# Optimization experiments

Measured on AMD Instinct MI355X. Metric: run time of the kernel, lower is better.

Reference implementation:

```python
import jax, jax.numpy as jnp
import numpy as np

N = 50000      # nodes
E = 800000     # edges
G = 256        # graphs in batch
D_IN = 128     # input_dim
H = 128        # node_hidden_dim
FC = 128       # fc_hidden_dim
OUT = 2        # out_dim
EPS = 1e-5


def _lin_init(key, fan_in, fan_out, bias=True):
    kw, kb = jax.random.split(key)
    w = jax.random.normal(kw, (fan_in, fan_out), jnp.float32) / np.sqrt(fan_in)
    if bias:
        b = jax.random.normal(kb, (fan_out,), jnp.float32) * 0.01
        return w, b
    return w


def setup_inputs() -> dict:
    key = jax.random.key(0)
    ks = jax.random.split(key, 16)
    x = jax.random.normal(ks[0], (N, D_IN), jnp.float32)
    edge_index = jax.random.randint(ks[1], (2, E), 0, N, jnp.int32)
    batch = jnp.sort(jax.random.randint(ks[2], (N,), 0, G, jnp.int32))
    edge_attr = jax.random.uniform(ks[3], (E, 1), jnp.float32)
    # GraphConv params: lin_rel (with bias) + lin_root (no bias)
    w_rel1, b_rel1 = _lin_init(ks[4], D_IN, H)
    w_root1 = _lin_init(ks[5], D_IN, H, bias=False)
    w_rel2, b_rel2 = _lin_init(ks[6], H, 2 * H)
    w_root2 = _lin_init(ks[7], H, 2 * H, bias=False)
    w_rel3, b_rel3 = _lin_init(ks[8], 2 * H, 3 * H)
    w_root3 = _lin_init(ks[9], 2 * H, 3 * H, bias=False)
    # BatchNorm affine params
    gamma1 = jnp.ones((H,), jnp.float32);      beta1 = jnp.zeros((H,), jnp.float32)
    gamma2 = jnp.ones((2 * H,), jnp.float32);  beta2 = jnp.zeros((2 * H,), jnp.float32)
    gamma3 = jnp.ones((3 * H,), jnp.float32);  beta3 = jnp.zeros((3 * H,), jnp.float32)
    # FC head: lin1 in = 3H+6H+9H = 18H
    w_lin1, b_lin1 = _lin_init(ks[10], 18 * H, FC)
    w_lin2, b_lin2 = _lin_init(ks[11], FC, OUT)
    w_lin3, b_lin3 = _lin_init(ks[12], OUT, OUT)
    return dict(x=x, edge_index=edge_index, batch=batch, edge_attr=edge_attr,
                w_rel1=w_rel1, b_rel1=b_rel1, w_root1=w_root1,
                w_rel2=w_rel2, b_rel2=b_rel2, w_root2=w_root2,
                w_rel3=w_rel3, b_rel3=b_rel3, w_root3=w_root3,
                gamma1=gamma1, beta1=beta1, gamma2=gamma2, beta2=beta2,
                gamma3=gamma3, beta3=beta3,
                w_lin1=w_lin1, b_lin1=b_lin1, w_lin2=w_lin2, b_lin2=b_lin2,
                w_lin3=w_lin3, b_lin3=b_lin3)


def _bn(h, gamma, beta):
    # training-mode BatchNorm1d over node axis
    mu = h.mean(0)
    var = h.var(0)
    return (h - mu) * jax.lax.rsqrt(var + EPS) * gamma + beta


def _gconv(h, src, dst, ew, w_rel, b_rel, w_root):
    # PyG GraphConv: lin_rel(sum_j ew_ij * x_j) + lin_root(x_i)
    agg = jax.ops.segment_sum(h[src] * ew[:, None], dst, num_segments=N)
    return agg @ w_rel + b_rel + h @ w_root


def _pool3(h, batch):
    # concat of global max / mean / add pooling per graph
    s = jax.ops.segment_sum(h, batch, num_segments=G)
    cnt = jax.ops.segment_sum(jnp.ones((h.shape[0], 1), h.dtype), batch, num_segments=G)
    mean = s / jnp.maximum(cnt, 1.0)
    m = jax.ops.segment_max(h, batch, num_segments=G)
    m = jnp.where(cnt > 0, m, 0.0)  # guard empty segments
    return jnp.concatenate([m, mean, s], axis=1)


def reference(x, edge_index, batch, edge_attr,
              w_rel1, b_rel1, w_root1, w_rel2, b_rel2, w_root2,
              w_rel3, b_rel3, w_root3,
              gamma1, beta1, gamma2, beta2, gamma3, beta3,
              w_lin1, b_lin1, w_lin2, b_lin2, w_lin3, b_lin3):
    ew = jnp.transpose(edge_attr, (1, 0))[0]            # [E]
    src, dst = edge_index[0], edge_index[1]
    h = _bn(jax.nn.leaky_relu(_gconv(x, src, dst, ew, w_rel1, b_rel1, w_root1)), gamma1, beta1)
    x1 = _pool3(h, batch)
    h = _bn(jax.nn.leaky_relu(_gconv(h, src, dst, ew, w_rel2, b_rel2, w_root2)), gamma2, beta2)
    x2 = _pool3(h, batch)
    h = _bn(jax.nn.leaky_relu(_gconv(h, src, dst, ew, w_rel3, b_rel3, w_root3)), gamma3, beta3)
    x3 = _pool3(h, batch)
    z = jnp.concatenate([x1, x2, x3], axis=1)           # [G, 18H]
    z = jax.nn.relu(z @ w_lin1 + b_lin1)                # dropout is identity in eval
    z = jax.nn.relu(z @ w_lin2 + b_lin2)
    return jax.nn.log_softmax(z @ w_lin3 + b_lin3, axis=-1)
```

## Files before the change

### kernel.cpp

```cpp
#include <hip/hip_runtime.h>
#include <cstdint>
#include <cstddef>

#define N_NODES 50000
#define M_PAD   50048
#define MB_TILES 391
#define N_EDGES 800000
#define N_GRAPH 256
#define Z_DIM   2304
#define NREP    16
#define POOL_TOT (N_GRAPH * (128 + 256 + 384))
#define PP_L1 (MB_TILES * 1 * 2 * 2 * 128)
#define PP_L2 (MB_TILES * 2 * 2 * 2 * 128)
#define PP_L3 (MB_TILES * 3 * 2 * 2 * 128)
#define PP_TOT (PP_L1 + PP_L2 + PP_L3)

static constexpr float LEAKY  = 0.01f;
static constexpr float BN_EPS = 1e-5f;
static constexpr float FNEG   = -3.4e38f;
static constexpr float FPOS   =  3.4e38f;

typedef short short8 __attribute__((ext_vector_type(8)));
typedef float floatx4 __attribute__((ext_vector_type(4)));
typedef const __attribute__((address_space(1))) unsigned int* gas_ptr;
typedef __attribute__((address_space(3))) unsigned int* las_ptr;
typedef unsigned long long ull;

__device__ __forceinline__ unsigned short f2b(float f) {
  union { float f; unsigned int u; } v; v.f = f;
  unsigned int u = v.u;
  unsigned int r = (u + 0x7FFFu + ((u >> 16) & 1u)) >> 16;
  return (unsigned short)r;
}
__device__ __forceinline__ float b2f(unsigned short h) {
  union { unsigned int u; float f; } v; v.u = ((unsigned int)h) << 16;
  return v.f;
}
__device__ __forceinline__ unsigned fkey(float x) {
  unsigned k = __float_as_uint(x);
  return k ^ ((k & 0x80000000u) ? 0xFFFFFFFFu : 0x80000000u);
}
__device__ __forceinline__ float kdec(unsigned k) {
  k ^= (k & 0x80000000u) ? 0x80000000u : 0xFFFFFFFFu;
  return __uint_as_float(k);
}


__global__ void init_all_kernel(int* __restrict__ cntR, int* __restrict__ gcnt,
                                float* __restrict__ sums_all,
                                unsigned* __restrict__ pmaxk, unsigned* __restrict__ pmink,
                                float* __restrict__ psumg) {
  const int i = blockIdx.x * blockDim.x + threadIdx.x;
  if (i < NREP * N_NODES) cntR[i] = 0;
  if (i < N_GRAPH) gcnt[i] = 0;
  if (i < 2 * (128 + 256 + 384)) sums_all[i] = 0.f;
  if (i < POOL_TOT) { pmaxk[i] = 0u; pmink[i] = 0xFFFFFFFFu; psumg[i] = 0.f; }
}


__global__ void hist_rep_kernel(const int* __restrict__ idx, int* __restrict__ cntR, int n) {
  int i = blockIdx.x * blockDim.x + threadIdx.x;
  if (i < n) {
    const int rep = blockIdx.x & (NREP - 1);
    atomicAdd(&cntR[rep * N_NODES + idx[i]], 1);
  }
}

__global__ __launch_bounds__(256) void scan1_fused_kernel(int* __restrict__ cntR,
                                                          int* __restrict__ out,
                                                          int* __restrict__ part, int n) {
  __shared__ int sm[256];
  const int t = threadIdx.x;
  const int base = blockIdx.x * 1024 + t * 4;
  int v[4] = {0, 0, 0, 0};
#pragma unroll
  for (int j = 0; j < 4; ++j) {
    const int d = base + j;
    if (d < n) {
      int s = 0;
#pragma unroll
      for (int r = 0; r < NREP; ++r) {
        const int c = cntR[r * N_NODES + d];
        cntR[r * N_NODES + d] = s;
        s += c;
      }
      v[j] = s;
    }
  }
  const int tsum = v[0] + v[1] + v[2] + v[3];
  sm[t] = tsum;
  __syncthreads();
  for (int off = 1; off < 256; off <<= 1) {
    int x = (t >= off) ? sm[t - off] : 0;
    __syncthreads();
    sm[t] += x;
    __syncthreads();
  }
  const int excl = sm[t] - tsum;
  if (base     < n) out[base]     = excl;
  if (base + 1 < n) out[base + 1] = excl + v[0];
  if (base + 2 < n) out[base + 2] = excl + v[0] + v[1];
  if (base + 3 < n) out[base + 3] = excl + v[0] + v[1] + v[2];
  if (t == 255) part[blockIdx.x] = sm[255];
}

__global__ __launch_bounds__(256) void scan2_kernel(int* __restrict__ part, int nb,
                                                    int* __restrict__ total_out) {
  __shared__ int sm[256];
  const int t = threadIdx.x;
  const int v = (t < nb) ? part[t] : 0;
  sm[t] = v;
  __syncthreads();
  for (int off = 1; off < 256; off <<= 1) {
    int x = (t >= off) ? sm[t - off] : 0;
    __syncthreads();
    sm[t] += x;
    __syncthreads();
  }
  if (t < nb) part[t] = sm[t] - v;
  if (t == 255) *total_out = sm[255];
}

__global__ void scan3_cursor_kernel(int* __restrict__ out, const int* __restrict__ part,
                                    int* __restrict__ cntR, int n) {
  int i = blockIdx.x * blockDim.x + threadIdx.x;
  if (i >= n) return;
  const int rp = out[i] + part[i >> 10];
  out[i] = rp;
#pragma unroll
  for (int r = 0; r < NREP; ++r) cntR[r * N_NODES + i] += rp;
}

__global__ void bucket_kernel(const int* __restrict__ src, const int* __restrict__ dst,
                              const float* __restrict__ ew, int* __restrict__ cntR,
                              ull* __restrict__ epack, int E) {
  int e = blockIdx.x * blockDim.x + threadIdx.x;
  if (e < E) {
    const int rep = blockIdx.x & (NREP - 1);
    const int d = dst[e];
    const int p = atomicAdd(&cntR[rep * N_NODES + d], 1);
    epack[p] = ((ull)__float_as_uint(ew[e]) << 32) | (unsigned)src[e];
  }
}

__global__ __launch_bounds__(256) void hist_batch_kernel(const int* __restrict__ idx,
                                                         int* __restrict__ cnt, int n) {
  __shared__ int lh[N_GRAPH];
  lh[threadIdx.x] = 0;
  __syncthreads();
  int i = blockIdx.x * blockDim.x + threadIdx.x;
  if (i < n) atomicAdd(&lh[idx[i]], 1);
  __syncthreads();
  const int v = lh[threadIdx.x];
  if (v) atomicAdd(&cnt[threadIdx.x], v);
}

__global__ __launch_bounds__(256) void scan256_kernel(const int* __restrict__ cnt,
                                                      int* __restrict__ gptr) {
  __shared__ int sm[256];
  const int t = threadIdx.x;
  const int v = cnt[t];
  sm[t] = v;
  __syncthreads();
  for (int off = 1; off < 256; off <<= 1) {
    int x = (t >= off) ? sm[t - off] : 0;
    __syncthreads();
    sm[t] += x;
    __syncthreads();
  }
  gptr[t] = sm[t] - v;
  if (t == 255) gptr[256] = sm[255];
}


__global__ void cast_bf16_kernel(const float* __restrict__ in,
                                 unsigned short* __restrict__ out, int npair) {
  int i = blockIdx.x * blockDim.x + threadIdx.x;
  if (i >= npair) return;
  float2 v = *(const float2*)(in + 2 * (size_t)i);
  ((unsigned int*)out)[i] = (unsigned int)f2b(v.x) | ((unsigned int)f2b(v.y) << 16);
}

__global__ __launch_bounds__(256) void wt_build_kernel(
    const float* __restrict__ wrel, const float* __restrict__ wroot,
    const float* __restrict__ brel, const float* __restrict__ sums_prev,
    const float* __restrict__ gamma_prev, const float* __restrict__ beta_prev,
    unsigned short* __restrict__ wt, float* __restrict__ u, float* __restrict__ v,
    int K, int N) {
  __shared__ float redu[256];
  __shared__ float redv[256];
  const int n = blockIdx.x;
  const int K2 = 2 * K;
  const float inv_n = 1.f / (float)N_NODES;
  float us = 0.f, vs = 0.f;
  for (int k = threadIdx.x; k < K2; k += 256) {
    const int kk = (k < K) ? k : k - K;
    const float w = (k < K) ? wrel[(size_t)kk * N + n] : wroot[(size_t)kk * N + n];
    float sc = 1.f, sh = 0.f;
    if (sums_prev) {
      const float mu  = sums_prev[kk] * inv_n;
      const float var = sums_prev[K + kk] * inv_n - mu * mu;
      sc = rsqrtf(var + BN_EPS) * gamma_prev[kk];
      sh = beta_prev[kk] - mu * sc;
    }
    wt[(size_t)n * K2 + k] = f2b(w * sc);
    if (k < K) us += sh * w; else vs += sh * w;
  }
  redu[threadIdx.x] = us; redv[threadIdx.x] = vs;
  __syncthreads();
  for (int o = 128; o > 0; o >>= 1) {
    if (threadIdx.x < o) {
      redu[threadIdx.x] += redu[threadIdx.x + o];
      redv[threadIdx.x] += redv[threadIdx.x + o];
    }
    __syncthreads();
  }
  if (threadIdx.x == 0) { u[n] = redu[0]; v[n] = brel[n] + redv[0]; }
}


template <int D>
__global__ void agg_bf16_kernel(const unsigned short* __restrict__ h,
                                const int* __restrict__ rowptr,
                                const ull* __restrict__ epack,
                                unsigned short* __restrict__ agg,
                                float* __restrict__ degw_out) {
  int gid  = blockIdx.x * blockDim.x + threadIdx.x;
  int node = gid >> 6;
  int lane = threadIdx.x & 63;
  if (node >= N_NODES) return;
  const int beg = rowptr[node], end = rowptr[node + 1];
  constexpr int NP = D / 128;
  float acc0[NP], acc1[NP];
#pragma unroll
  for (int i = 0; i < NP; ++i) { acc0[i] = 0.f; acc1[i] = 0.f; }
  float wsum = 0.f;

  for (int c0 = beg; c0 < end; c0 += 64) {
    const int cn = min(64, end - c0);
    ull pk = 0;
    if (lane < cn) pk = epack[c0 + lane];
    const int   su = (int)(unsigned)pk;
    const float wf = __uint_as_float((unsigned)(pk >> 32));
    const int ng = (cn + 7) >> 3;
    for (int g = 0; g < ng; ++g) {
      int ss[8]; float wv[8];
#pragma unroll
      for (int j = 0; j < 8; ++j) {
        ss[j] = __shfl(su, g * 8 + j);
        wv[j] = __shfl(wf, g * 8 + j);
      }
      unsigned uu[8][NP];
#pragma unroll
      for (int j = 0; j < 8; ++j) {
        const unsigned int* row = (const unsigned int*)(h + (size_t)ss[j] * D);
#pragma unroll
        for (int i = 0; i < NP; ++i) uu[j][i] = row[lane + 64 * i];
      }
#pragma unroll
      for (int j = 0; j < 8; ++j) {
        wsum += wv[j];
#pragma unroll
        for (int i = 0; i < NP; ++i) {
          acc0[i] += b2f((unsigned short)(uu[j][i] & 0xFFFF)) * wv[j];
          acc1[i] += b2f((unsigned short)(uu[j][i] >> 16)) * wv[j];
        }
      }
    }
  }

  unsigned int* o = (unsigned int*)(agg + (size_t)node * D);
#pragma unroll
  for (int i = 0; i < NP; ++i)
    o[lane + 64 * i] = (unsigned int)f2b(acc0[i]) | ((unsigned int)f2b(acc1[i]) << 16);
  if (degw_out != nullptr && lane == 0) degw_out[node] = wsum;
}


__global__ __launch_bounds__(256) void gemm_mfma_kernel(
    const unsigned short* __restrict__ Aagg, const unsigned short* __restrict__ Ah,
    const unsigned short* __restrict__ Wt,
    const float* __restrict__ u, const float* __restrict__ v,
    const float* __restrict__ degw, const int* __restrict__ batch,
    unsigned short* __restrict__ outH, float* __restrict__ sums,
    unsigned* __restrict__ pmaxk, unsigned* __restrict__ pmink,
    float* __restrict__ psumg,
    float* __restrict__ ppmax, float* __restrict__ ppmin, float* __restrict__ ppsum,
    int M, int K, int N) {
  __shared__ unsigned short As[3][128 * 32];
  __shared__ unsigned short Bs[3][128 * 32];
  __shared__ float col_s[256];
  __shared__ float dws[128];
  __shared__ int gbs[128];

  const int NT = N >> 7;
  const int id = blockIdx.x;
  const int xcd = id & 7;
  const int q   = id >> 3;
  const int m_tile = (q / NT) * 8 + xcd;
  if (m_tile >= MB_TILES) return;
  const int m0 = m_tile * 128;
  const int nt2 = q % NT;
  const int n0 = nt2 * 128;

  const int t  = threadIdx.x;
  const int lane = t & 63;
  const int w    = t >> 6;
  const int wm   = (w & 1) * 64;
  const int wn   = (w >> 1) * 64;
  const int l16  = lane & 15;
  const int lq   = lane >> 4;
  const int K2   = 2 * K;

  const int lrow  = lane >> 2;
  const int lslot = lane & 3;

  col_s[t] = 0.f;
  if (t < 128) {
    const int m = m0 + t;
    dws[t] = (m < M) ? degw[m] : 0.f;
    gbs[t] = (m < M) ? batch[m] : -1;
  }

  floatx4 acc[4][4];
#pragma unroll
  for (int i = 0; i < 4; ++i)
#pragma unroll
    for (int j = 0; j < 4; ++j) acc[i][j] = (floatx4){0.f, 0.f, 0.f, 0.f};

  auto stage = [&](unsigned short* Ab, unsigned short* Bb, int k0) {
    const unsigned short* Asrc;
    int kbase;
    if (k0 < K) { Asrc = Aagg; kbase = k0; } else { Asrc = Ah; kbase = k0 - K; }
#pragma unroll
    for (int qq = 0; qq < 2; ++qq) {
      const int row = w * 32 + qq * 16 + lrow;
      const int gc  = (lslot ^ ((row >> 1) & 3)) * 8;
      const unsigned short* gA = Asrc + (size_t)(m0 + row) * K + kbase + gc;
      const unsigned short* gB = Wt + (size_t)(n0 + row) * K2 + k0 + gc;
      __builtin_amdgcn_global_load_lds((gas_ptr)gA, (las_ptr)(Ab + (w * 32 + qq * 16) * 32),
                                       16, 0, 0);
      __builtin_amdgcn_global_load_lds((gas_ptr)gB, (las_ptr)(Bb + (w * 32 + qq * 16) * 32),
                                       16, 0, 0);
    }
  };

  auto compute = [&](const unsigned short* Ab, const unsigned short* Bb) {
    short8 af[4], bfr[4];
#pragma unroll
    for (int i = 0; i < 4; ++i) {
      const int r = wm + i * 16 + l16;
      af[i] = *(const short8*)(Ab + r * 32 + (lq ^ ((r >> 1) & 3)) * 8);
    }
#pragma unroll
    for (int j = 0; j < 4; ++j) {
      const int r = wn + j * 16 + l16;
      bfr[j] = *(const short8*)(Bb + r * 32 + (lq ^ ((r >> 1) & 3)) * 8);
    }
    __builtin_amdgcn_s_setprio(1);
#pragma unroll
    for (int i = 0; i < 4; ++i)
#pragma unroll
      for (int j = 0; j < 4; ++j)
        acc[i][j] = __builtin_amdgcn_mfma_f32_16x16x32_bf16(af[i], bfr[j], acc[i][j], 0, 0, 0);
    __builtin_amdgcn_s_setprio(0);
  };

  const int NSTEP = K2 >> 5;

  unsigned short *A0 = &As[0][0], *A1 = &As[1][0], *A2 = &As[2][0];
  unsigned short *B0 = &Bs[0][0], *B1 = &Bs[1][0], *B2 = &Bs[2][0];

  stage(A0, B0, 0);
  stage(A1, B1, 1 << 5);

  for (int s = 0; s < NSTEP - 1; ++s) {
    asm volatile("s_waitcnt vmcnt(4)" ::: "memory");
    __builtin_amdgcn_s_barrier();
    __builtin_amdgcn_sched_barrier(0);
    if (s + 2 < NSTEP) stage(A2, B2, (s + 2) << 5);
    compute(A0, B0);
    unsigned short* tA = A0; A0 = A1; A1 = A2; A2 = tA;
    unsigned short* tB = B0; B0 = B1; B1 = B2; B2 = tB;
  }
  asm volatile("s_waitcnt vmcnt(0)" ::: "memory");
  __builtin_amdgcn_s_barrier();
  __builtin_amdgcn_sched_barrier(0);
  compute(A0, B0);

  float uu[4], vv[4];
#pragma unroll
  for (int j = 0; j < 4; ++j) {
    const int n = n0 + wn + j * 16 + l16;
    uu[j] = u[n]; vv[j] = v[n];
  }

  const bool wout = (outH != nullptr);
  const int lastr = min(127, M - 1 - m0);
  const int gmin = gbs[0];
  const int gmax = gbs[lastr];

  float ts[4]  = {0.f, 0.f, 0.f, 0.f};
  float tss[4] = {0.f, 0.f, 0.f, 0.f};
  float px0[4], pn0[4], ps0[4], px1[4], pn1[4], ps1[4];
#pragma unroll
  for (int j = 0; j < 4; ++j) {
    px0[j] = FNEG; pn0[j] = FPOS; ps0[j] = 0.f;
    px1[j] = FNEG; pn1[j] = FPOS; ps1[j] = 0.f;
  }

#pragma unroll
  for (int i = 0; i < 4; ++i) {
    const int lrow2 = wm + i * 16 + lq * 4;
#pragma unroll
    for (int r = 0; r < 4; ++r) {
      const int row = lrow2 + r;
      const bool live = (m0 + row < M);
      const int gv = gbs[row];
      const float dwr = dws[row];
      const bool in0 = live && (gv == gmin);
      const bool in1 = live && (gmax != gmin) && (gv == gmax);
#pragma unroll
      for (int j = 0; j < 4; ++j) {
        const int n = n0 + wn + j * 16 + l16;
        float val = acc[i][j][r] + vv[j] + dwr * uu[j];
        val = val > 0.f ? val : LEAKY * val;
        acc[i][j][r] = val;
        if (live) {
          if (wout) outH[(size_t)(m0 + row) * N + n] = f2b(val);
          ts[j]  += val;
          tss[j] += val * val;
        }
        if (in0) { px0[j] = fmaxf(px0[j], val); pn0[j] = fminf(pn0[j], val); ps0[j] += val; }
        if (in1) { px1[j] = fmaxf(px1[j], val); pn1[j] = fminf(pn1[j], val); ps1[j] += val; }
      }
    }
  }

  const int half = w & 1;
#pragma unroll
  for (int j = 0; j < 4; ++j) {
    float a = ts[j], b = tss[j];
    a += __shfl_xor(a, 16); a += __shfl_xor(a, 32);
    b += __shfl_xor(b, 16); b += __shfl_xor(b, 32);
    float x0 = px0[j], n0v = pn0[j], s0v = ps0[j];
    x0 = fmaxf(x0, __shfl_xor(x0, 16)); x0 = fmaxf(x0, __shfl_xor(x0, 32));
    n0v = fminf(n0v, __shfl_xor(n0v, 16)); n0v = fminf(n0v, __shfl_xor(n0v, 32));
    s0v += __shfl_xor(s0v, 16); s0v += __shfl_xor(s0v, 32);
    float x1 = px1[j], n1v = pn1[j], s1v = ps1[j];
    x1 = fmaxf(x1, __shfl_xor(x1, 16)); x1 = fmaxf(x1, __shfl_xor(x1, 32));
    n1v = fminf(n1v, __shfl_xor(n1v, 16)); n1v = fminf(n1v, __shfl_xor(n1v, 32));
    s1v += __shfl_xor(s1v, 16); s1v += __shfl_xor(s1v, 32);
    if (lq == 0) {
      const int ci = wn + j * 16 + l16;
      atomicAdd(&col_s[ci], a);
      atomicAdd(&col_s[128 + ci], b);
      const size_t tb = (size_t)(m_tile * NT + nt2) * 2;
      const size_t sb0 = ((tb + 0) * 2 + half) * 128 + ci;
      const size_t sb1 = ((tb + 1) * 2 + half) * 128 + ci;
      ppmax[sb0] = x0;  ppmin[sb0] = n0v; ppsum[sb0] = s0v;
      ppmax[sb1] = x1;  ppmin[sb1] = n1v; ppsum[sb1] = s1v;
    }
  }

  if (gmax > gmin + 1) {
    for (int g = gmin + 1; g < gmax; ++g) {
#pragma unroll
      for (int j = 0; j < 4; ++j) {
        float mx = FNEG, mn = FPOS, sm = 0.f;
#pragma unroll
        for (int i = 0; i < 4; ++i) {
          const int lrow2 = wm + i * 16 + lq * 4;
#pragma unroll
          for (int r = 0; r < 4; ++r) {
            const int row = lrow2 + r;
            if (m0 + row < M && gbs[row] == g) {
              const float val = acc[i][j][r];
              mx = fmaxf(mx, val); mn = fminf(mn, val); sm += val;
            }
          }
        }
        mx = fmaxf(mx, __shfl_xor(mx, 16)); mx = fmaxf(mx, __shfl_xor(mx, 32));
        mn = fminf(mn, __shfl_xor(mn, 16)); mn = fminf(mn, __shfl_xor(mn, 32));
        sm += __shfl_xor(sm, 16); sm += __shfl_xor(sm, 32);
        if (lq == 0 && mx > -3.3e38f) {
          const size_t pi = (size_t)g * N + (n0 + wn + j * 16 + l16);
          atomicMax(&pmaxk[pi], fkey(mx));
          atomicMin(&pmink[pi], fkey(mn));
          atomicAdd(&psumg[pi], sm);
        }
      }
    }
  }

  __syncthreads();
  if (t < 128) {
    atomicAdd(&sums[n0 + t], col_s[t]);
    atomicAdd(&sums[N + n0 + t], col_s[128 + t]);
  }
}


__global__ void pool_finalize_all_kernel(const unsigned* __restrict__ pmaxk,
                                         const unsigned* __restrict__ pmink,
                                         const float* __restrict__ psumg,
                                         const float* __restrict__ ppmax,
                                         const float* __restrict__ ppmin,
                                         const float* __restrict__ ppsum,
                                         const float* __restrict__ sums_all,
                                         const float* __restrict__ gamma1, const float* __restrict__ beta1,
                                         const float* __restrict__ gamma2, const float* __restrict__ beta2,
                                         const float* __restrict__ gamma3, const float* __restrict__ beta3,
                                         const int* __restrict__ gptr,
                                         const int* __restrict__ batch,
                                         float* __restrict__ z) {
  int i = blockIdx.x * blockDim.x + threadIdx.x;
  if (i >= POOL_TOT) return;
  int C, zoff, li, NTL;
  size_t ppo;
  const float *sums, *gamma, *beta;
  if (i < N_GRAPH * 128) {
    C = 128; zoff = 0; li = i; NTL = 1; ppo = 0;
    sums = sums_all; gamma = gamma1; beta = beta1;
  } else if (i < N_GRAPH * (128 + 256)) {
    C = 256; zoff = 384; li = i - N_GRAPH * 128; NTL = 2; ppo = PP_L1;
    sums = sums_all + 2 * 128; gamma = gamma2; beta = beta2;
  } else {
    C = 384; zoff = 1152; li = i - N_GRAPH * (128 + 256); NTL = 3; ppo = PP_L1 + PP_L2;
    sums = sums_all + 2 * (128 + 256); gamma = gamma3; beta = beta3;
  }
  const int g = li / C, c = li % C;
  const int cnt = gptr[g + 1] - gptr[g];

  float mx = FNEG, mn = FPOS, sm = psumg[i];
  {
    const unsigned pk = pmaxk[i];
    if (pk != 0u) mx = kdec(pk);
    const unsigned nk = pmink[i];
    if (nk != 0xFFFFFFFFu) mn = kdec(nk);
  }
  if (cnt > 0) {
    const int mt_lo = gptr[g] >> 7;
    const int mt_hi = (gptr[g + 1] - 1) >> 7;
    const int nt = c >> 7, cc = c & 127;
    for (int mt = mt_lo; mt <= mt_hi; ++mt) {
      const int g0 = batch[mt << 7];
      int grel = (g == g0) ? 0 : -1;
      if (grel < 0) {
        const int lastm = min((mt << 7) + 127, N_NODES - 1);
        if (g == batch[lastm]) grel = 1;
      }
      if (grel >= 0) {
        const size_t b0 = ppo + (((size_t)(mt * NTL + nt) * 2 + grel) * 2 + 0) * 128 + cc;
        const size_t b1 = b0 + 128;
        mx = fmaxf(mx, fmaxf(ppmax[b0], ppmax[b1]));
        mn = fminf(mn, fminf(ppmin[b0], ppmin[b1]));
        sm += ppsum[b0] + ppsum[b1];
      }
    }
  }

  const float inv_n = 1.f / (float)N_NODES;
  const float mu  = sums[c] * inv_n;
  const float var = sums[C + c] * inv_n - mu * mu;
  const float sc  = rsqrtf(var + BN_EPS) * gamma[c];
  const float sh  = beta[c] - mu * sc;
  const float zmax = (sc >= 0.f ? mx : mn) * sc + sh;
  const float zsum = sm * sc + (float)cnt * sh;
  float* zg = z + (size_t)g * Z_DIM + zoff;
  zg[c]         = (cnt > 0) ? zmax : 0.f;
  zg[C + c]     = zsum / (float)(cnt > 0 ? cnt : 1);
  zg[2 * C + c] = zsum;
}


__global__ __launch_bounds__(1024) void fc_kernel(const float* __restrict__ z,
                                                  const float* __restrict__ w1, const float* __restrict__ b1,
                                                  const float* __restrict__ w2, const float* __restrict__ b2,
                                                  const float* __restrict__ w3, const float* __restrict__ b3,
                                                  float* __restrict__ out) {
  __shared__ float zs[Z_DIM];
  __shared__ float part[8][128];
  __shared__ float h1s[128];
  __shared__ float red[128][2];
  __shared__ float y2[2];
  const int g  = blockIdx.x;
  const int t  = threadIdx.x;
  const int c  = t & 127;
  const int ks = t >> 7;
  for (int i = t; i < Z_DIM; i += 1024) zs[i] = z[(size_t)g * Z_DIM + i];
  __syncthreads();

  constexpr int KCH = Z_DIM / 8;
  const int k0 = ks * KCH;
  float acc = 0.f;
#pragma unroll 4
  for (int k = k0; k < k0 + KCH; ++k) acc += zs[k] * w1[(size_t)k * 128 + c];
  part[ks][c] = acc;
  __syncthreads();

  if (t < 128) {
    float s = b1[t];
#pragma unroll
    for (int i = 0; i < 8; ++i) s += part[i][t];
    h1s[t] = fmaxf(s, 0.f);
  }
  __syncthreads();
  if (t < 128) {
    red[t][0] = h1s[t] * w2[t * 2 + 0];
    red[t][1] = h1s[t] * w2[t * 2 + 1];
  }
  __syncthreads();
  if (t < 2) {
    float s = b2[t];
    for (int k = 0; k < 128; ++k) s += red[k][t];
    y2[t] = fmaxf(s, 0.f);
  }
  __syncthreads();
  if (t == 0) {
    const float z0 = y2[0] * w3[0] + y2[1] * w3[2] + b3[0];
    const float z1 = y2[0] * w3[1] + y2[1] * w3[3] + b3[1];
    const float m  = fmaxf(z0, z1);
    const float lse = m + logf(expf(z0 - m) + expf(z1 - m));
    out[g * 2 + 0] = z0 - lse;
    out[g * 2 + 1] = z1 - lse;
  }
}


extern "C" void kernel_launch(void* const* d_in, const int* in_sizes, int n_in,
                              void* d_out, int out_size, void* d_ws, size_t ws_size,
                              hipStream_t stream) {
  (void)in_sizes; (void)n_in; (void)out_size; (void)ws_size;
  const float* x        = (const float*)d_in[0];
  const int*   eidx     = (const int*)d_in[1];
  const int*   batch    = (const int*)d_in[2];
  const float* eattr    = (const float*)d_in[3];
  const float* w_rel1   = (const float*)d_in[4];
  const float* b_rel1   = (const float*)d_in[5];
  const float* w_root1  = (const float*)d_in[6];
  const float* w_rel2   = (const float*)d_in[7];
  const float* b_rel2   = (const float*)d_in[8];
  const float* w_root2  = (const float*)d_in[9];
  const float* w_rel3   = (const float*)d_in[10];
  const float* b_rel3   = (const float*)d_in[11];
  const float* w_root3  = (const float*)d_in[12];
  const float* gamma1   = (const float*)d_in[13];
  const float* beta1    = (const float*)d_in[14];
  const float* gamma2   = (const float*)d_in[15];
  const float* beta2    = (const float*)d_in[16];
  const float* gamma3   = (const float*)d_in[17];
  const float* beta3    = (const float*)d_in[18];
  const float* w_lin1   = (const float*)d_in[19];
  const float* b_lin1   = (const float*)d_in[20];
  const float* w_lin2   = (const float*)d_in[21];
  const float* b_lin2   = (const float*)d_in[22];
  const float* w_lin3   = (const float*)d_in[23];
  const float* b_lin3   = (const float*)d_in[24];

  const int* src = eidx;
  const int* dst = eidx + N_EDGES;
  float* outp = (float*)d_out;

  char* ws = (char*)d_ws;
  size_t off = 0;
  auto alloc = [&](size_t bytes) -> void* {
    void* p = ws + off;
    off += (bytes + 255) & ~(size_t)255;
    return p;
  };
  int*   rowptr = (int*)alloc((N_NODES + 1) * sizeof(int));
  int*   cntR   = (int*)alloc((size_t)NREP * N_NODES * sizeof(int));
  int*   gptr   = (int*)alloc((N_GRAPH + 1) * sizeof(int));
  int*   gcnt   = (int*)alloc(N_GRAPH * sizeof(int));
  int*   part   = (int*)alloc(256 * sizeof(int));
  ull*   epack  = (ull*)alloc((size_t)N_EDGES * sizeof(ull));
  float* degw   = (float*)alloc(N_NODES * sizeof(float));
  float* sums_all = (float*)alloc(2 * (128 + 256 + 384) * sizeof(float));
  float* zbuf   = (float*)alloc((size_t)N_GRAPH * Z_DIM * sizeof(float));
  unsigned* pmaxk = (unsigned*)alloc((size_t)POOL_TOT * 4);
  unsigned* pmink = (unsigned*)alloc((size_t)POOL_TOT * 4);
  float*    psumg = (float*)alloc((size_t)POOL_TOT * 4);
  float* ppmax = (float*)alloc((size_t)PP_TOT * 4);
  float* ppmin = (float*)alloc((size_t)PP_TOT * 4);
  float* ppsum = (float*)alloc((size_t)PP_TOT * 4);
  unsigned short* xb   = (unsigned short*)alloc((size_t)M_PAD * 128 * 2);
  unsigned short* hp1  = (unsigned short*)alloc((size_t)M_PAD * 128 * 2);
  unsigned short* hp2  = (unsigned short*)alloc((size_t)M_PAD * 256 * 2);
  unsigned short* aggb = (unsigned short*)alloc((size_t)M_PAD * 256 * 2);
  unsigned short* wt1 = (unsigned short*)alloc((size_t)128 * 256 * 2);
  unsigned short* wt2 = (unsigned short*)alloc((size_t)256 * 256 * 2);
  unsigned short* wt3 = (unsigned short*)alloc((size_t)384 * 512 * 2);
  float* u1 = (float*)alloc(128 * sizeof(float));
  float* v1 = (float*)alloc(128 * sizeof(float));
  float* u2 = (float*)alloc(256 * sizeof(float));
  float* v2 = (float*)alloc(256 * sizeof(float));
  float* u3 = (float*)alloc(384 * sizeof(float));
  float* v3 = (float*)alloc(384 * sizeof(float));

  float* sums1 = sums_all;
  float* sums2 = sums_all + 2 * 128;
  float* sums3 = sums_all + 2 * (128 + 256);
  const int PO1 = 0, PO2 = N_GRAPH * 128, PO3 = N_GRAPH * (128 + 256);

  const int EB = (N_EDGES + 255) / 256;
  const int NB = (N_NODES + 255) / 256;
  const int SB = (N_NODES + 1023) / 1024;

  init_all_kernel<<<(NREP * N_NODES + 255) / 256, 256, 0, stream>>>(
      cntR, gcnt, sums_all, pmaxk, pmink, psumg);

  hist_rep_kernel<<<EB, 256, 0, stream>>>(dst, cntR, N_EDGES);
  scan1_fused_kernel<<<SB, 256, 0, stream>>>(cntR, rowptr, part, N_NODES);
  scan2_kernel<<<1, 256, 0, stream>>>(part, SB, rowptr + N_NODES);
  scan3_cursor_kernel<<<NB, 256, 0, stream>>>(rowptr, part, cntR, N_NODES);
  bucket_kernel<<<EB, 256, 0, stream>>>(src, dst, eattr, cntR, epack, N_EDGES);

  hist_batch_kernel<<<NB, 256, 0, stream>>>(batch, gcnt, N_NODES);
  scan256_kernel<<<1, 256, 0, stream>>>(gcnt, gptr);

  cast_bf16_kernel<<<(N_NODES * 128 / 2 + 255) / 256, 256, 0, stream>>>(x, xb, N_NODES * 128 / 2);
  wt_build_kernel<<<128, 256, 0, stream>>>(w_rel1, w_root1, b_rel1, nullptr, nullptr, nullptr,
                                           wt1, u1, v1, 128, 128);

  const int aggBlocks = (N_NODES * 64 + 255) / 256;

  agg_bf16_kernel<128><<<aggBlocks, 256, 0, stream>>>(xb, rowptr, epack, aggb, degw);
  gemm_mfma_kernel<<<392 * 1, 256, 0, stream>>>(aggb, xb, wt1, u1, v1, degw, batch,
                                                hp1, sums1, pmaxk + PO1, pmink + PO1,
                                                psumg + PO1, ppmax, ppmin, ppsum,
                                                N_NODES, 128, 128);
  wt_build_kernel<<<256, 256, 0, stream>>>(w_rel2, w_root2, b_rel2, sums1, gamma1, beta1,
                                           wt2, u2, v2, 128, 256);

  agg_bf16_kernel<128><<<aggBlocks, 256, 0, stream>>>(hp1, rowptr, epack, aggb, nullptr);
  gemm_mfma_kernel<<<392 * 2, 256, 0, stream>>>(aggb, hp1, wt2, u2, v2, degw, batch,
                                                hp2, sums2, pmaxk + PO2, pmink + PO2,
                                                psumg + PO2, ppmax + PP_L1, ppmin + PP_L1,
                                                ppsum + PP_L1, N_NODES, 128, 256);
  wt_build_kernel<<<384, 256, 0, stream>>>(w_rel3, w_root3, b_rel3, sums2, gamma2, beta2,
                                           wt3, u3, v3, 256, 384);

  agg_bf16_kernel<256><<<aggBlocks, 256, 0, stream>>>(hp2, rowptr, epack, aggb, nullptr);
  gemm_mfma_kernel<<<392 * 3, 256, 0, stream>>>(aggb, hp2, wt3, u3, v3, degw, batch,
                                                (unsigned short*)nullptr, sums3,
                                                pmaxk + PO3, pmink + PO3, psumg + PO3,
                                                ppmax + PP_L1 + PP_L2, ppmin + PP_L1 + PP_L2,
                                                ppsum + PP_L1 + PP_L2, N_NODES, 256, 384);

  pool_finalize_all_kernel<<<(POOL_TOT + 255) / 256, 256, 0, stream>>>(
      pmaxk, pmink, psumg, ppmax, ppmin, ppsum, sums_all,
      gamma1, beta1, gamma2, beta2, gamma3, beta3, gptr, batch, zbuf);
  fc_kernel<<<N_GRAPH, 1024, 0, stream>>>(zbuf, w_lin1, b_lin1, w_lin2, b_lin2, w_lin3, b_lin3,
                                          outp);
}
```

Before: 502.7 us.

## Load GEMM fragments directly from global into registers, drop LDS staging

The MFMA GEMM no longer stages A and B tiles through a triple-buffered LDS pipeline with global_load_lds and barriers. Each wave now loads its short8 fragments straight from global memory into registers, double-buffered in software, and sets a launch-bounds occupancy hint of 3. This removes LDS traffic and per-step barriers and frees LDS for more resident blocks. In exchange, rows shared between waves are loaded redundantly, the global accesses are less coalesced, and register pressure rises, which may cap occupancy. A __syncthreads was also added after the shared-memory init, fixing a latent race left when the loop barriers were removed.

```diff
diff --git a/kernel.cpp b/kernel.cpp
--- a/kernel.cpp
+++ b/kernel.cpp
@@ -22,8 +22,6 @@
 
 typedef short short8 __attribute__((ext_vector_type(8)));
 typedef float floatx4 __attribute__((ext_vector_type(4)));
-typedef const __attribute__((address_space(1))) unsigned int* gas_ptr;
-typedef __attribute__((address_space(3))) unsigned int* las_ptr;
 typedef unsigned long long ull;
 
 __device__ __forceinline__ unsigned short f2b(float f) {
@@ -277,7 +275,7 @@
 }
 
 
-__global__ __launch_bounds__(256) void gemm_mfma_kernel(
+__global__ __launch_bounds__(256, 3) void gemm_mfma_kernel(
     const unsigned short* __restrict__ Aagg, const unsigned short* __restrict__ Ah,
     const unsigned short* __restrict__ Wt,
     const float* __restrict__ u, const float* __restrict__ v,
@@ -287,8 +285,6 @@
     float* __restrict__ psumg,
     float* __restrict__ ppmax, float* __restrict__ ppmin, float* __restrict__ ppsum,
     int M, int K, int N) {
-  __shared__ unsigned short As[3][128 * 32];
-  __shared__ unsigned short Bs[3][128 * 32];
   __shared__ float col_s[256];
   __shared__ float dws[128];
   __shared__ int gbs[128];
@@ -312,15 +308,13 @@
   const int lq   = lane >> 4;
   const int K2   = 2 * K;
 
-  const int lrow  = lane >> 2;
-  const int lslot = lane & 3;
-
   col_s[t] = 0.f;
   if (t < 128) {
     const int m = m0 + t;
     dws[t] = (m < M) ? degw[m] : 0.f;
     gbs[t] = (m < M) ? batch[m] : -1;
   }
+  __syncthreads();
 
   floatx4 acc[4][4];
 #pragma unroll
@@ -328,65 +322,42 @@
 #pragma unroll
     for (int j = 0; j < 4; ++j) acc[i][j] = (floatx4){0.f, 0.f, 0.f, 0.f};
 
-  auto stage = [&](unsigned short* Ab, unsigned short* Bb, int k0) {
-    const unsigned short* Asrc;
-    int kbase;
-    if (k0 < K) { Asrc = Aagg; kbase = k0; } else { Asrc = Ah; kbase = k0 - K; }
-#pragma unroll
-    for (int qq = 0; qq < 2; ++qq) {
-      const int row = w * 32 + qq * 16 + lrow;
-      const int gc  = (lslot ^ ((row >> 1) & 3)) * 8;
-      const unsigned short* gA = Asrc + (size_t)(m0 + row) * K + kbase + gc;
-      const unsigned short* gB = Wt + (size_t)(n0 + row) * K2 + k0 + gc;
-      __builtin_amdgcn_global_load_lds((gas_ptr)gA, (las_ptr)(Ab + (w * 32 + qq * 16) * 32),
-                                       16, 0, 0);
-      __builtin_amdgcn_global_load_lds((gas_ptr)gB, (las_ptr)(Bb + (w * 32 + qq * 16) * 32),
-                                       16, 0, 0);
-    }
+  const unsigned short* ApA = Aagg + (size_t)(m0 + wm + l16) * K + lq * 8;
+  const unsigned short* ApH = Ah   + (size_t)(m0 + wm + l16) * K + lq * 8;
+  const unsigned short* Bp  = Wt   + (size_t)(n0 + wn + l16) * K2 + lq * 8;
+
+  short8 afA[4], bfA[4], afB[4], bfB[4];
+
+  auto loadf = [&](short8* af, short8* bf, int s) {
+    const int k0 = s << 5;
+    const unsigned short* Ap = (k0 < K) ? (ApA + k0) : (ApH + (k0 - K));
+#pragma unroll
+    for (int i = 0; i < 4; ++i)
+      af[i] = *(const short8*)(Ap + (size_t)(i * 16) * K);
+    const unsigned short* Bq = Bp + k0;
+#pragma unroll
+    for (int j = 0; j < 4; ++j)
+      bf[j] = *(const short8*)(Bq + (size_t)(j * 16) * K2);
   };
-
-  auto compute = [&](const unsigned short* Ab, const unsigned short* Bb) {
-    short8 af[4], bfr[4];
-#pragma unroll
-    for (int i = 0; i < 4; ++i) {
-      const int r = wm + i * 16 + l16;
-      af[i] = *(const short8*)(Ab + r * 32 + (lq ^ ((r >> 1) & 3)) * 8);
-    }
-#pragma unroll
-    for (int j = 0; j < 4; ++j) {
-      const int r = wn + j * 16 + l16;
-      bfr[j] = *(const short8*)(Bb + r * 32 + (lq ^ ((r >> 1) & 3)) * 8);
-    }
+  auto mf16 = [&](short8* af, short8* bf) {
     __builtin_amdgcn_s_setprio(1);
 #pragma unroll
     for (int i = 0; i < 4; ++i)
 #pragma unroll
       for (int j = 0; j < 4; ++j)
-        acc[i][j] = __builtin_amdgcn_mfma_f32_16x16x32_bf16(af[i], bfr[j], acc[i][j], 0, 0, 0);
+        acc[i][j] = __builtin_amdgcn_mfma_f32_16x16x32_bf16(af[i], bf[j], acc[i][j], 0, 0, 0);
     __builtin_amdgcn_s_setprio(0);
   };
 
   const int NSTEP = K2 >> 5;
 
-  unsigned short *A0 = &As[0][0], *A1 = &As[1][0], *A2 = &As[2][0];
-  unsigned short *B0 = &Bs[0][0], *B1 = &Bs[1][0], *B2 = &Bs[2][0];
-
-  stage(A0, B0, 0);
-  stage(A1, B1, 1 << 5);
-
-  for (int s = 0; s < NSTEP - 1; ++s) {
-    asm volatile("s_waitcnt vmcnt(4)" ::: "memory");
-    __builtin_amdgcn_s_barrier();
-    __builtin_amdgcn_sched_barrier(0);
-    if (s + 2 < NSTEP) stage(A2, B2, (s + 2) << 5);
-    compute(A0, B0);
-    unsigned short* tA = A0; A0 = A1; A1 = A2; A2 = tA;
-    unsigned short* tB = B0; B0 = B1; B1 = B2; B2 = tB;
-  }
-  asm volatile("s_waitcnt vmcnt(0)" ::: "memory");
-  __builtin_amdgcn_s_barrier();
-  __builtin_amdgcn_sched_barrier(0);
-  compute(A0, B0);
+  loadf(afA, bfA, 0);
+  for (int s = 0; s < NSTEP; s += 2) {
+    loadf(afB, bfB, s + 1);
+    mf16(afA, bfA);
+    if (s + 2 < NSTEP) loadf(afA, bfA, s + 2);
+    mf16(afB, bfB);
+  }
 
   float uu[4], vv[4];
 #pragma unroll
@@ -451,7 +422,7 @@
     x1 = fmaxf(x1, __shfl_xor(x1, 16)); x1 = fmaxf(x1, __shfl_xor(x1, 32));
     n1v = fminf(n1v, __shfl_xor(n1v, 16)); n1v = fminf(n1v, __shfl_xor(n1v, 32));
     s1v += __shfl_xor(s1v, 16); s1v += __shfl_xor(s1v, 32);
-    if (lq == 0) {
+    if (lane < 16) {
       const int ci = wn + j * 16 + l16;
       atomicAdd(&col_s[ci], a);
       atomicAdd(&col_s[128 + ci], b);
@@ -483,7 +454,7 @@
         mx = fmaxf(mx, __shfl_xor(mx, 16)); mx = fmaxf(mx, __shfl_xor(mx, 32));
         mn = fminf(mn, __shfl_xor(mn, 16)); mn = fminf(mn, __shfl_xor(mn, 32));
         sm += __shfl_xor(sm, 16); sm += __shfl_xor(sm, 32);
-        if (lq == 0 && mx > -3.3e38f) {
+        if (lane < 16 && mx > -3.3e38f) {
           const size_t pi = (size_t)g * N + (n0 + wn + j * 16 + l16);
           atomicMax(&pmaxk[pi], fkey(mx));
           atomicMin(&pmink[pi], fkey(mn));
```

Result: slower. 553.3 us (+10.1%).

## Shrink GEMM LDS footprint: double-buffer B, alias epilogue scratch onto tile buffers

Applied to the files above, without the earlier changes.

Keeps A triple-buffered but cuts the B weight tile to two buffers, staging B one step ahead instead of two. The epilogue scratch arrays (col_s, dws, gbs) now alias the tile buffers in one 40 KB shared array and are filled after the main loop behind extra barriers. The goal is lower LDS use per block so more blocks fit per CU. In exchange B loads get less latency slack, and the epilogue adds two __syncthreads plus a dependent load of degw and batch after the MFMA loop.

```diff
diff --git a/kernel.cpp b/kernel.cpp
--- a/kernel.cpp
+++ b/kernel.cpp
@@ -287,11 +287,12 @@
     float* __restrict__ psumg,
     float* __restrict__ ppmax, float* __restrict__ ppmin, float* __restrict__ ppsum,
     int M, int K, int N) {
-  __shared__ unsigned short As[3][128 * 32];
-  __shared__ unsigned short Bs[3][128 * 32];
-  __shared__ float col_s[256];
-  __shared__ float dws[128];
-  __shared__ int gbs[128];
+  __shared__ char smem[40960];
+  unsigned short* AsBase = (unsigned short*)smem;
+  unsigned short* BsBase = (unsigned short*)(smem + 24576);
+  float* col_s = (float*)smem;
+  float* dws   = (float*)(smem + 1024);
+  int*   gbs   = (int*)(smem + 1536);
 
   const int NT = N >> 7;
   const int id = blockIdx.x;
@@ -315,78 +316,89 @@
   const int lrow  = lane >> 2;
   const int lslot = lane & 3;
 
+  floatx4 acc[4][4];
+#pragma unroll
+  for (int i = 0; i < 4; ++i)
+#pragma unroll
+    for (int j = 0; j < 4; ++j) acc[i][j] = (floatx4){0.f, 0.f, 0.f, 0.f};
+
+  auto stage_A = [&](unsigned short* Ab, int k0) {
+    const unsigned short* Asrc;
+    int kbase;
+    if (k0 < K) { Asrc = Aagg; kbase = k0; } else { Asrc = Ah; kbase = k0 - K; }
+#pragma unroll
+    for (int qq = 0; qq < 2; ++qq) {
+      const int row = w * 32 + qq * 16 + lrow;
+      const int gc  = (lslot ^ ((row >> 1) & 3)) * 8;
+      const unsigned short* gA = Asrc + (size_t)(m0 + row) * K + kbase + gc;
+      __builtin_amdgcn_global_load_lds((gas_ptr)gA, (las_ptr)(Ab + (w * 32 + qq * 16) * 32),
+                                       16, 0, 0);
+    }
+  };
+  auto stage_B = [&](unsigned short* Bb, int k0) {
+#pragma unroll
+    for (int qq = 0; qq < 2; ++qq) {
+      const int row = w * 32 + qq * 16 + lrow;
+      const int gc  = (lslot ^ ((row >> 1) & 3)) * 8;
+      const unsigned short* gB = Wt + (size_t)(n0 + row) * K2 + k0 + gc;
+      __builtin_amdgcn_global_load_lds((gas_ptr)gB, (las_ptr)(Bb + (w * 32 + qq * 16) * 32),
+                                       16, 0, 0);
+    }
+  };
+
+  auto compute = [&](const unsigned short* Ab, const unsigned short* Bb) {
+    short8 af[4], bfr[4];
+#pragma unroll
+    for (int i = 0; i < 4; ++i) {
+      const int r = wm + i * 16 + l16;
+      af[i] = *(const short8*)(Ab + r * 32 + (lq ^ ((r >> 1) & 3)) * 8);
+    }
+#pragma unroll
+    for (int j = 0; j < 4; ++j) {
+      const int r = wn + j * 16 + l16;
+      bfr[j] = *(const short8*)(Bb + r * 32 + (lq ^ ((r >> 1) & 3)) * 8);
+    }
+    __builtin_amdgcn_s_setprio(1);
+#pragma unroll
+    for (int i = 0; i < 4; ++i)
+#pragma unroll
+      for (int j = 0; j < 4; ++j)
+        acc[i][j] = __builtin_amdgcn_mfma_f32_16x16x32_bf16(af[i], bfr[j], acc[i][j], 0, 0, 0);
+    __builtin_amdgcn_s_setprio(0);
+  };
+
+  const int NSTEP = K2 >> 5;
+
+  unsigned short *A0 = AsBase, *A1 = AsBase + 4096, *A2 = AsBase + 8192;
+  unsigned short *B0 = BsBase, *B1 = BsBase + 4096;
+
+  stage_A(A0, 0);
+  stage_B(B0, 0);
+  stage_A(A1, 1 << 5);
+
+  for (int s = 0; s < NSTEP - 1; ++s) {
+    asm volatile("s_waitcnt vmcnt(2)" ::: "memory");
+    __builtin_amdgcn_s_barrier();
+    __builtin_amdgcn_sched_barrier(0);
+    stage_B(B1, (s + 1) << 5);
+    if (s + 2 < NSTEP) stage_A(A2, (s + 2) << 5);
+    compute(A0, B0);
+    unsigned short* tA = A0; A0 = A1; A1 = A2; A2 = tA;
+    unsigned short* tB = B0; B0 = B1; B1 = tB;
+  }
+  asm volatile("s_waitcnt vmcnt(0)" ::: "memory");
+  __builtin_amdgcn_s_barrier();
+  __builtin_amdgcn_sched_barrier(0);
+  compute(A0, B0);
+
+  __syncthreads();
   col_s[t] = 0.f;
   if (t < 128) {
     const int m = m0 + t;
     dws[t] = (m < M) ? degw[m] : 0.f;
     gbs[t] = (m < M) ? batch[m] : -1;
   }
-
-  floatx4 acc[4][4];
-#pragma unroll
-  for (int i = 0; i < 4; ++i)
-#pragma unroll
-    for (int j = 0; j < 4; ++j) acc[i][j] = (floatx4){0.f, 0.f, 0.f, 0.f};
-
-  auto stage = [&](unsigned short* Ab, unsigned short* Bb, int k0) {
-    const unsigned short* Asrc;
-    int kbase;
-    if (k0 < K) { Asrc = Aagg; kbase = k0; } else { Asrc = Ah; kbase = k0 - K; }
-#pragma unroll
-    for (int qq = 0; qq < 2; ++qq) {
-      const int row = w * 32 + qq * 16 + lrow;
-      const int gc  = (lslot ^ ((row >> 1) & 3)) * 8;
-      const unsigned short* gA = Asrc + (size_t)(m0 + row) * K + kbase + gc;
-      const unsigned short* gB = Wt + (size_t)(n0 + row) * K2 + k0 + gc;
-      __builtin_amdgcn_global_load_lds((gas_ptr)gA, (las_ptr)(Ab + (w * 32 + qq * 16) * 32),
-                                       16, 0, 0);
-      __builtin_amdgcn_global_load_lds((gas_ptr)gB, (las_ptr)(Bb + (w * 32 + qq * 16) * 32),
-                                       16, 0, 0);
-    }
-  };
-
-  auto compute = [&](const unsigned short* Ab, const unsigned short* Bb) {
-    short8 af[4], bfr[4];
-#pragma unroll
-    for (int i = 0; i < 4; ++i) {
-      const int r = wm + i * 16 + l16;
-      af[i] = *(const short8*)(Ab + r * 32 + (lq ^ ((r >> 1) & 3)) * 8);
-    }
-#pragma unroll
-    for (int j = 0; j < 4; ++j) {
-      const int r = wn + j * 16 + l16;
-      bfr[j] = *(const short8*)(Bb + r * 32 + (lq ^ ((r >> 1) & 3)) * 8);
-    }
-    __builtin_amdgcn_s_setprio(1);
-#pragma unroll
-    for (int i = 0; i < 4; ++i)
-#pragma unroll
-      for (int j = 0; j < 4; ++j)
-        acc[i][j] = __builtin_amdgcn_mfma_f32_16x16x32_bf16(af[i], bfr[j], acc[i][j], 0, 0, 0);
-    __builtin_amdgcn_s_setprio(0);
-  };
-
-  const int NSTEP = K2 >> 5;
-
-  unsigned short *A0 = &As[0][0], *A1 = &As[1][0], *A2 = &As[2][0];
-  unsigned short *B0 = &Bs[0][0], *B1 = &Bs[1][0], *B2 = &Bs[2][0];
-
-  stage(A0, B0, 0);
-  stage(A1, B1, 1 << 5);
-
-  for (int s = 0; s < NSTEP - 1; ++s) {
-    asm volatile("s_waitcnt vmcnt(4)" ::: "memory");
-    __builtin_amdgcn_s_barrier();
-    __builtin_amdgcn_sched_barrier(0);
-    if (s + 2 < NSTEP) stage(A2, B2, (s + 2) << 5);
-    compute(A0, B0);
-    unsigned short* tA = A0; A0 = A1; A1 = A2; A2 = tA;
-    unsigned short* tB = B0; B0 = B1; B1 = B2; B2 = tB;
-  }
-  asm volatile("s_waitcnt vmcnt(0)" ::: "memory");
-  __builtin_amdgcn_s_barrier();
-  __builtin_amdgcn_sched_barrier(0);
-  compute(A0, B0);
+  __syncthreads();
 
   float uu[4], vv[4];
 #pragma unroll
```

New measurement: 499.7 us. Within noise of the previous version (-0.6%).
